# Kernel tuning notes

Hardware: AMD Instinct MI355X
Metric: run time of the kernel (lower is better)

Reference implementation:

```python
import jax, jax.numpy as jnp
import numpy as np

D_MODEL = 1024
N_HEAD = 16
D_K = D_MODEL // N_HEAD


def setup_inputs() -> dict:
    key = jax.random.key(0)
    k1, k2, k3 = jax.random.split(key, 3)
    B, S = 2, 2048
    x = jax.random.normal(k1, (B, S, D_MODEL), dtype=jnp.float32)
    attention_mask = jnp.ones((B, 1, 1, S), dtype=jnp.float32)
    # Conv1D params: weight [nx, nf], bias [nf]; init std=0.02 per source
    W_attn = 0.02 * jax.random.normal(k2, (D_MODEL, 3 * D_MODEL), dtype=jnp.float32)
    b_attn = jnp.zeros((3 * D_MODEL,), dtype=jnp.float32)
    W_proj = 0.02 * jax.random.normal(k3, (D_MODEL, D_MODEL), dtype=jnp.float32)
    b_proj = jnp.zeros((D_MODEL,), dtype=jnp.float32)
    return {"x": x, "attention_mask": attention_mask,
            "W_attn": W_attn, "b_attn": b_attn,
            "W_proj": W_proj, "b_proj": b_proj}


def reference(x, attention_mask, W_attn, b_attn, W_proj, b_proj):
    B, S, _ = x.shape
    # c_attn: fused QKV projection (Conv1D == addmm)
    qkv = x @ W_attn + b_attn                       # [B, S, 3*D]
    q, k, v = jnp.split(qkv, 3, axis=-1)            # each [B, S, D]

    def split_heads(t):                             # [B, S, D] -> [B, H, S, d_k]
        return t.reshape(B, S, N_HEAD, D_K).transpose(0, 2, 1, 3)

    q, k, v = split_heads(q), split_heads(k), split_heads(v)
    scale = 1.0 / jnp.sqrt(jnp.float32(D_K))
    scores = jnp.einsum("bhqd,bhkd->bhqk", q, k) * scale   # [B, H, S, S]
    scores = scores + (1.0 - attention_mask) * -10000.0
    scores = jax.nn.softmax(scores, axis=-1)
    # dropout omitted (eval / deterministic)
    out = jnp.einsum("bhqk,bhkd->bhqd", scores, v)          # [B, H, S, d_k]
    out = out.transpose(0, 2, 1, 3).reshape(B, S, D_MODEL)  # merge heads
    out = out @ W_proj + b_proj                             # c_proj
    return out, scores
```

## Files before the change

### kernel.cpp

```cpp
#include <hip/hip_runtime.h>

typedef unsigned short u16;
typedef __bf16 bf16x8 __attribute__((ext_vector_type(8)));
typedef float f32x4 __attribute__((ext_vector_type(4)));

#define D_MODEL 1024
#define S_LEN 2048
#define NH 16
#define DK 64
#define BATCH 2
#define M_ROWS (BATCH * S_LEN)
#define NQKV (3 * D_MODEL)

__device__ __forceinline__ u16 f2bf(float x) {
  union { __bf16 h; u16 u; } v; v.h = (__bf16)x;
  return v.u;
}
__device__ __forceinline__ float bf2f(u16 b) {
  union { unsigned u; float f; } v; v.u = ((unsigned)b) << 16; return v.f;
}
__device__ __forceinline__ void gload16(const void* g, void* l) {
  __builtin_amdgcn_global_load_lds((const __attribute__((address_space(1))) unsigned int*)g,
                                   (__attribute__((address_space(3))) unsigned int*)l, 16, 0, 0);
}

__global__ __launch_bounds__(256) void pack_bf16(const float* __restrict__ in, u16* __restrict__ out) {
  const int idx = (blockIdx.x * 256 + threadIdx.x) * 8;
  float4 a = *(const float4*)&in[idx];
  float4 b = *(const float4*)&in[idx + 4];
  unsigned p0 = (unsigned)f2bf(a.x) | ((unsigned)f2bf(a.y) << 16);
  unsigned p1 = (unsigned)f2bf(a.z) | ((unsigned)f2bf(a.w) << 16);
  unsigned p2 = (unsigned)f2bf(b.x) | ((unsigned)f2bf(b.y) << 16);
  unsigned p3 = (unsigned)f2bf(b.z) | ((unsigned)f2bf(b.w) << 16);
  int4 o; o.x = (int)p0; o.y = (int)p1; o.z = (int)p2; o.w = (int)p3;
  *(int4*)&out[idx] = o;
}

__global__ __launch_bounds__(256) void transpose_pack(const float* __restrict__ in, u16* __restrict__ out,
                                                      int R, int C) {
  __shared__ u16 T[64][68];
  const int r0 = blockIdx.x * 64, c0 = blockIdx.y * 64;
  const int t = threadIdx.x;
  const int col = t & 63, rq = t >> 6;
#pragma unroll
  for (int s = 0; s < 16; ++s) {
    int row = s * 4 + rq;
    T[col][row] = f2bf(in[(size_t)(r0 + row) * C + c0 + col]);
  }
  __syncthreads();
#pragma unroll
  for (int s = 0; s < 16; ++s) {
    int crow = s * 4 + rq;
    out[(size_t)(c0 + crow) * R + r0 + col] = T[crow][col];
  }
}

template <int OUTF32>
__global__ __launch_bounds__(256) void gemm_bt(const u16* __restrict__ A, const u16* __restrict__ BT,
                                               const float* __restrict__ bias, void* __restrict__ outp,
                                               int K, int N) {
  __shared__ u16 As[2][128 * 64];
  __shared__ u16 Bs[2][128 * 64];
  const int m0 = blockIdx.x * 128, n0 = blockIdx.y * 128;
  const int t = threadIdx.x, lane = t & 63, w = t >> 6;
  const int wr = w >> 1, wc = w & 1;
  const int l15 = lane & 15, l4 = lane >> 4;
  const int srow = lane >> 3, schunk = lane & 7;

  f32x4 acc[4][4] = {};

#define STAGE_G(buf, k0)                                                        \
  do {                                                                          \
    _Pragma("unroll") for (int i = 0; i < 4; ++i) {                             \
      int r0 = (i * 4 + w) * 8;                                                 \
      int r = r0 + srow;                                                        \
      int sc = (schunk ^ (r & 7)) * 8;                                          \
      gload16(&A[(size_t)(m0 + r) * K + (k0) + sc], &As[buf][r0 * 64]);         \
      gload16(&BT[(size_t)(n0 + r) * K + (k0) + sc], &Bs[buf][r0 * 64]);        \
    }                                                                           \
  } while (0)

  STAGE_G(0, 0);
  __syncthreads();
  const int nk = K / 64;
  int cur = 0;
  for (int t0 = 0; t0 < nk; ++t0) {
    if (t0 + 1 < nk) STAGE_G(cur ^ 1, (t0 + 1) * 64);
#pragma unroll
    for (int ks = 0; ks < 2; ++ks) {
      bf16x8 af[4], bfr[4];
#pragma unroll
      for (int g = 0; g < 4; ++g) {
        int ra = wr * 64 + g * 16 + l15;
        int rb = wc * 64 + g * 16 + l15;
        af[g]  = *(const bf16x8*)&As[cur][ra * 64 + ((ks * 4 + l4) ^ (ra & 7)) * 8];
        bfr[g] = *(const bf16x8*)&Bs[cur][rb * 64 + ((ks * 4 + l4) ^ (rb & 7)) * 8];
      }
#pragma unroll
      for (int mg = 0; mg < 4; ++mg)
#pragma unroll
        for (int ng = 0; ng < 4; ++ng)
          acc[mg][ng] = __builtin_amdgcn_mfma_f32_16x16x32_bf16(af[mg], bfr[ng], acc[mg][ng], 0, 0, 0);
    }
    __syncthreads();
    cur ^= 1;
  }
#undef STAGE_G
  const int rowb = m0 + wr * 64, colb = n0 + wc * 64;
#pragma unroll
  for (int mg = 0; mg < 4; ++mg)
#pragma unroll
    for (int ng = 0; ng < 4; ++ng) {
      int col = colb + ng * 16 + l15;
      float bv = bias[col];
#pragma unroll
      for (int j = 0; j < 4; ++j) {
        int row = rowb + mg * 16 + l4 * 4 + j;
        float val = acc[mg][ng][j] + bv;
        if (OUTF32) ((float*)outp)[(size_t)row * N + col] = val;
        else        ((u16*)outp)[(size_t)row * N + col] = f2bf(val);
      }
    }
}

__global__ __launch_bounds__(512, 6) void attn_fused(const u16* __restrict__ qkv, const float* __restrict__ mask,
                                                     float* __restrict__ scores, u16* __restrict__ attnout) {
  __shared__ u16 Ks[2][64 * 64];
  __shared__ u16 Vt[2][64 * 68];
  __shared__ u16 Ps[8][16][40];
  __shared__ float RS[4][16][2];
  const int bid = blockIdx.x;
  const int qt = bid & 31, h = (bid >> 5) & 15, b = bid >> 9;
  const int t = threadIdx.x, lane = t & 63, w = t >> 6;
  const int qg = w >> 1, kg = w & 1;
  const int l15 = lane & 15, l4 = lane >> 4;
  const u16* kbase = qkv + (size_t)b * S_LEN * NQKV + D_MODEL + h * DK;
  const u16* vbase = kbase + D_MODEL;
  const float* mrow = mask + b * S_LEN;

  bf16x8 qf[2];
  {
    const int qrow = qt * 64 + qg * 16 + l15;
    const u16* qp = qkv + (size_t)(b * S_LEN + qrow) * NQKV + h * DK;
#pragma unroll
    for (int ks = 0; ks < 2; ++ks) {
      union { bf16x8 v; u16 s[8]; } qa;
      qa.v = *(const bf16x8*)&qp[ks * 32 + l4 * 8];
#pragma unroll
      for (int e = 0; e < 8; ++e) qa.s[e] = f2bf(bf2f(qa.s[e]) * 0.125f);
      qf[ks] = qa.v;
    }
  }

  const int krow = t >> 3;
  const int kchunk = ((t & 7) ^ (krow & 7)) * 8;
#define STAGE_K(buf, kt) \
  gload16(&kbase[(size_t)((kt) * 64 + krow) * NQKV + kchunk], &Ks[buf][w * 512])

  float ps4[4] = {0.f, 0.f, 0.f, 0.f};
  int cur = 0;
  STAGE_K(0, 0);
  __syncthreads();
  for (int kt = 0; kt < 32; ++kt) {
    if (kt + 1 < 32) STAGE_K(cur ^ 1, kt + 1);
    f32x4 sacc[2] = {};
#pragma unroll
    for (int ks = 0; ks < 2; ++ks) {
      bf16x8 kf[2];
#pragma unroll
      for (int n = 0; n < 2; ++n) {
        int kr = kg * 32 + n * 16 + l15;
        kf[n] = *(const bf16x8*)&Ks[cur][kr * 64 + ((ks * 4 + l4) ^ (kr & 7)) * 8];
      }
#pragma unroll
      for (int n = 0; n < 2; ++n)
        sacc[n] = __builtin_amdgcn_mfma_f32_16x16x32_bf16(qf[ks], kf[n], sacc[n], 0, 0, 0);
    }
#pragma unroll
    for (int n = 0; n < 2; ++n) {
      float m = mrow[kt * 64 + kg * 32 + n * 16 + l15];
      float mb = -10000.0f * (1.0f - m);
#pragma unroll
      for (int j = 0; j < 4; ++j) ps4[j] += __expf(sacc[n][j] + mb);
    }
    __syncthreads();
    cur ^= 1;
  }
#pragma unroll
  for (int off = 1; off < 16; off <<= 1)
#pragma unroll
    for (int j = 0; j < 4; ++j) ps4[j] += __shfl_xor(ps4[j], off, 64);
  if (l15 == 0)
#pragma unroll
    for (int j = 0; j < 4; ++j) RS[qg][l4 * 4 + j][kg] = ps4[j];
  __syncthreads();
  float inv4[4];
#pragma unroll
  for (int j = 0; j < 4; ++j) inv4[j] = 1.0f / (RS[qg][l4 * 4 + j][0] + RS[qg][l4 * 4 + j][1]);

  f32x4 oacc[4] = {};
  const int vr = t >> 3, vc = (t & 7) * 8;
  const size_t sbase = ((size_t)((b * NH + h) * S_LEN + qt * 64 + qg * 16 + l4 * 4)) * S_LEN + l15;

  STAGE_K(0, 0);
  {
    const u16* vp = &vbase[(size_t)vr * NQKV + vc];
    int4 va0 = *(const int4*)vp;
    const u16* s0 = (const u16*)&va0;
#pragma unroll
    for (int i = 0; i < 8; ++i) Vt[0][(vc + i) * 68 + vr] = s0[i];
  }
  __syncthreads();
  cur = 0;
  for (int kt = 0; kt < 32; ++kt) {
    const bool hn = (kt + 1 < 32);
    int4 va;
    if (hn) {
      STAGE_K(cur ^ 1, kt + 1);
      va = *(const int4*)&vbase[(size_t)((kt + 1) * 64 + vr) * NQKV + vc];
    }
    f32x4 sacc[2] = {};
#pragma unroll
    for (int ks = 0; ks < 2; ++ks) {
      bf16x8 kf[2];
#pragma unroll
      for (int n = 0; n < 2; ++n) {
        int kr = kg * 32 + n * 16 + l15;
        kf[n] = *(const bf16x8*)&Ks[cur][kr * 64 + ((ks * 4 + l4) ^ (kr & 7)) * 8];
      }
#pragma unroll
      for (int n = 0; n < 2; ++n)
        sacc[n] = __builtin_amdgcn_mfma_f32_16x16x32_bf16(qf[ks], kf[n], sacc[n], 0, 0, 0);
    }
#pragma unroll
    for (int n = 0; n < 2; ++n) {
      float m = mrow[kt * 64 + kg * 32 + n * 16 + l15];
      float mb = -10000.0f * (1.0f - m);
#pragma unroll
      for (int j = 0; j < 4; ++j) {
        float p = __expf(sacc[n][j] + mb) * inv4[j];
        scores[sbase + (size_t)j * S_LEN + kt * 64 + kg * 32 + n * 16] = p;
        Ps[w][l4 * 4 + j][n * 16 + l15] = f2bf(p);
      }
    }
    {
      bf16x8 pa = *(const bf16x8*)&Ps[w][l15][l4 * 8];
      bf16x8 vf[4];
#pragma unroll
      for (int dn = 0; dn < 4; ++dn)
        vf[dn] = *(const bf16x8*)&Vt[cur][(dn * 16 + l15) * 68 + kg * 32 + l4 * 8];
#pragma unroll
      for (int dn = 0; dn < 4; ++dn)
        oacc[dn] = __builtin_amdgcn_mfma_f32_16x16x32_bf16(pa, vf[dn], oacc[dn], 0, 0, 0);
    }
    if (hn) {
      const u16* s0 = (const u16*)&va;
#pragma unroll
      for (int i = 0; i < 8; ++i) Vt[cur ^ 1][(vc + i) * 68 + vr] = s0[i];
    }
    __syncthreads();
    cur ^= 1;
  }
#undef STAGE_K
  float* OX = (float*)&Ks[0][0];
  if (kg == 1) {
#pragma unroll
    for (int dn = 0; dn < 4; ++dn)
#pragma unroll
      for (int j = 0; j < 4; ++j)
        OX[(qg * 16 + l4 * 4 + j) * 64 + dn * 16 + l15] = oacc[dn][j];
  }
  __syncthreads();
  if (kg == 0) {
#pragma unroll
    for (int dn = 0; dn < 4; ++dn) {
      int col = h * DK + dn * 16 + l15;
#pragma unroll
      for (int j = 0; j < 4; ++j) {
        int row = b * S_LEN + qt * 64 + qg * 16 + l4 * 4 + j;
        float o = oacc[dn][j] + OX[(qg * 16 + l4 * 4 + j) * 64 + dn * 16 + l15];
        attnout[(size_t)row * D_MODEL + col] = f2bf(o);
      }
    }
  }
}

extern "C" void kernel_launch(void* const* d_in, const int* in_sizes, int n_in,
                              void* d_out, int out_size, void* d_ws, size_t ws_size,
                              hipStream_t stream) {
  const float* x      = (const float*)d_in[0];
  const float* mask   = (const float*)d_in[1];
  const float* W_attn = (const float*)d_in[2];
  const float* b_attn = (const float*)d_in[3];
  const float* W_proj = (const float*)d_in[4];
  const float* b_proj = (const float*)d_in[5];
  float* out    = (float*)d_out;
  float* scores = out + (size_t)M_ROWS * D_MODEL;

  char* ws = (char*)d_ws;
  u16* xb     = (u16*)ws;
  u16* wqkvT  = (u16*)(ws + (size_t)(8  << 20));
  u16* wprojT = (u16*)(ws + (size_t)(14 << 20));
  u16* qkv    = (u16*)(ws + (size_t)(16 << 20));
  u16* attnb  = (u16*)(ws + (size_t)(40 << 20));

  pack_bf16<<<(M_ROWS * D_MODEL) / (256 * 8), 256, 0, stream>>>(x, xb);
  transpose_pack<<<dim3(D_MODEL / 64, NQKV / 64), 256, 0, stream>>>(W_attn, wqkvT, D_MODEL, NQKV);
  transpose_pack<<<dim3(D_MODEL / 64, D_MODEL / 64), 256, 0, stream>>>(W_proj, wprojT, D_MODEL, D_MODEL);
  gemm_bt<0><<<dim3(M_ROWS / 128, NQKV / 128), 256, 0, stream>>>(xb, wqkvT, b_attn, (void*)qkv, D_MODEL, NQKV);
  attn_fused<<<BATCH * NH * (S_LEN / 64), 512, 0, stream>>>(qkv, mask, scores, attnb);
  gemm_bt<1><<<dim3(M_ROWS / 128, D_MODEL / 128), 256, 0, stream>>>(attnb, wprojT, b_proj, (void*)out, D_MODEL, D_MODEL);
}
```

Before: 287.4 us.

## Double attention query tile per block, precompute mask bias in LDS

Each attention block now handles 128 query rows instead of 64, with each wave computing two 16-row MFMA groups. This halves the number of K/V tile loads and V transposes per query row. The mask bias is precomputed once into shared memory instead of being read from global memory every iteration. The end-of-loop __syncthreads is replaced with an explicit lgkmcnt wait plus a raw barrier. In exchange it uses more registers and LDS, lowers the occupancy target to 4, and halves the grid to 512 blocks.

```diff
diff --git a/kernel.cpp b/kernel.cpp
--- a/kernel.cpp
+++ b/kernel.cpp
@@ -123,24 +123,33 @@
     }
 }
 
-__global__ __launch_bounds__(512, 6) void attn_fused(const u16* __restrict__ qkv, const float* __restrict__ mask,
+__global__ __launch_bounds__(512, 4) void attn_fused(const u16* __restrict__ qkv, const float* __restrict__ mask,
                                                      float* __restrict__ scores, u16* __restrict__ attnout) {
   __shared__ u16 Ks[2][64 * 64];
   __shared__ u16 Vt[2][64 * 68];
-  __shared__ u16 Ps[8][16][40];
-  __shared__ float RS[4][16][2];
+  __shared__ u16 Ps[8][32][40];
+  __shared__ float MB[S_LEN];
+  __shared__ float RS[4][32][2];
   const int bid = blockIdx.x;
-  const int qt = bid & 31, h = (bid >> 5) & 15, b = bid >> 9;
+  const int qt = bid & 15, h = (bid >> 4) & 15, b = bid >> 8;
   const int t = threadIdx.x, lane = t & 63, w = t >> 6;
   const int qg = w >> 1, kg = w & 1;
   const int l15 = lane & 15, l4 = lane >> 4;
   const u16* kbase = qkv + (size_t)b * S_LEN * NQKV + D_MODEL + h * DK;
   const u16* vbase = kbase + D_MODEL;
-  const float* mrow = mask + b * S_LEN;
-
-  bf16x8 qf[2];
+
   {
-    const int qrow = qt * 64 + qg * 16 + l15;
+    float4 m4 = *(const float4*)&mask[b * S_LEN + t * 4];
+    MB[t * 4 + 0] = -10000.0f * (1.0f - m4.x);
+    MB[t * 4 + 1] = -10000.0f * (1.0f - m4.y);
+    MB[t * 4 + 2] = -10000.0f * (1.0f - m4.z);
+    MB[t * 4 + 3] = -10000.0f * (1.0f - m4.w);
+  }
+
+  bf16x8 qf[2][2];
+#pragma unroll
+  for (int mg = 0; mg < 2; ++mg) {
+    const int qrow = qt * 128 + qg * 32 + mg * 16 + l15;
     const u16* qp = qkv + (size_t)(b * S_LEN + qrow) * NQKV + h * DK;
 #pragma unroll
     for (int ks = 0; ks < 2; ++ks) {
@@ -148,22 +157,22 @@
       qa.v = *(const bf16x8*)&qp[ks * 32 + l4 * 8];
 #pragma unroll
       for (int e = 0; e < 8; ++e) qa.s[e] = f2bf(bf2f(qa.s[e]) * 0.125f);
-      qf[ks] = qa.v;
-    }
-  }
-
-  const int krow = t >> 3;
-  const int kchunk = ((t & 7) ^ (krow & 7)) * 8;
+      qf[mg][ks] = qa.v;
+    }
+  }
+
+  const int krow = w * 8 + (lane >> 3);
+  const int kchunk = ((lane & 7) ^ (krow & 7)) * 8;
 #define STAGE_K(buf, kt) \
   gload16(&kbase[(size_t)((kt) * 64 + krow) * NQKV + kchunk], &Ks[buf][w * 512])
 
-  float ps4[4] = {0.f, 0.f, 0.f, 0.f};
+  float ps4[2][4] = {};
   int cur = 0;
   STAGE_K(0, 0);
   __syncthreads();
   for (int kt = 0; kt < 32; ++kt) {
     if (kt + 1 < 32) STAGE_K(cur ^ 1, kt + 1);
-    f32x4 sacc[2] = {};
+    f32x4 sacc[2][2] = {};
 #pragma unroll
     for (int ks = 0; ks < 2; ++ks) {
       bf16x8 kf[2];
@@ -173,15 +182,18 @@
         kf[n] = *(const bf16x8*)&Ks[cur][kr * 64 + ((ks * 4 + l4) ^ (kr & 7)) * 8];
       }
 #pragma unroll
-      for (int n = 0; n < 2; ++n)
-        sacc[n] = __builtin_amdgcn_mfma_f32_16x16x32_bf16(qf[ks], kf[n], sacc[n], 0, 0, 0);
+      for (int mg = 0; mg < 2; ++mg)
+#pragma unroll
+        for (int n = 0; n < 2; ++n)
+          sacc[mg][n] = __builtin_amdgcn_mfma_f32_16x16x32_bf16(qf[mg][ks], kf[n], sacc[mg][n], 0, 0, 0);
     }
 #pragma unroll
     for (int n = 0; n < 2; ++n) {
-      float m = mrow[kt * 64 + kg * 32 + n * 16 + l15];
-      float mb = -10000.0f * (1.0f - m);
-#pragma unroll
-      for (int j = 0; j < 4; ++j) ps4[j] += __expf(sacc[n][j] + mb);
+      float mb = MB[kt * 64 + kg * 32 + n * 16 + l15];
+#pragma unroll
+      for (int mg = 0; mg < 2; ++mg)
+#pragma unroll
+        for (int j = 0; j < 4; ++j) ps4[mg][j] += __expf(sacc[mg][n][j] + mb);
     }
     __syncthreads();
     cur ^= 1;
@@ -189,18 +201,31 @@
 #pragma unroll
   for (int off = 1; off < 16; off <<= 1)
 #pragma unroll
-    for (int j = 0; j < 4; ++j) ps4[j] += __shfl_xor(ps4[j], off, 64);
+    for (int mg = 0; mg < 2; ++mg)
+#pragma unroll
+      for (int j = 0; j < 4; ++j) ps4[mg][j] += __shfl_xor(ps4[mg][j], off, 64);
   if (l15 == 0)
 #pragma unroll
-    for (int j = 0; j < 4; ++j) RS[qg][l4 * 4 + j][kg] = ps4[j];
-  __syncthreads();
-  float inv4[4];
-#pragma unroll
-  for (int j = 0; j < 4; ++j) inv4[j] = 1.0f / (RS[qg][l4 * 4 + j][0] + RS[qg][l4 * 4 + j][1]);
-
-  f32x4 oacc[4] = {};
+    for (int mg = 0; mg < 2; ++mg)
+#pragma unroll
+      for (int j = 0; j < 4; ++j) RS[qg][mg * 16 + l4 * 4 + j][kg] = ps4[mg][j];
+  __syncthreads();
+  float inv4[2][4];
+#pragma unroll
+  for (int mg = 0; mg < 2; ++mg)
+#pragma unroll
+    for (int j = 0; j < 4; ++j) {
+      int r = mg * 16 + l4 * 4 + j;
+      inv4[mg][j] = 1.0f / (RS[qg][r][0] + RS[qg][r][1]);
+    }
+
+  f32x4 oacc[2][4] = {};
   const int vr = t >> 3, vc = (t & 7) * 8;
-  const size_t sbase = ((size_t)((b * NH + h) * S_LEN + qt * 64 + qg * 16 + l4 * 4)) * S_LEN + l15;
+  size_t sb[2];
+#pragma unroll
+  for (int mg = 0; mg < 2; ++mg)
+    sb[mg] = ((size_t)((b * NH + h) * S_LEN + qt * 128 + qg * 32 + mg * 16 + l4 * 4)) * S_LEN
+             + kg * 32 + l15;
 
   STAGE_K(0, 0);
   {
@@ -219,7 +244,7 @@
       STAGE_K(cur ^ 1, kt + 1);
       va = *(const int4*)&vbase[(size_t)((kt + 1) * 64 + vr) * NQKV + vc];
     }
-    f32x4 sacc[2] = {};
+    f32x4 sacc[2][2] = {};
 #pragma unroll
     for (int ks = 0; ks < 2; ++ks) {
       bf16x8 kf[2];
@@ -229,59 +254,75 @@
         kf[n] = *(const bf16x8*)&Ks[cur][kr * 64 + ((ks * 4 + l4) ^ (kr & 7)) * 8];
       }
 #pragma unroll
-      for (int n = 0; n < 2; ++n)
-        sacc[n] = __builtin_amdgcn_mfma_f32_16x16x32_bf16(qf[ks], kf[n], sacc[n], 0, 0, 0);
+      for (int mg = 0; mg < 2; ++mg)
+#pragma unroll
+        for (int n = 0; n < 2; ++n)
+          sacc[mg][n] = __builtin_amdgcn_mfma_f32_16x16x32_bf16(qf[mg][ks], kf[n], sacc[mg][n], 0, 0, 0);
     }
 #pragma unroll
     for (int n = 0; n < 2; ++n) {
-      float m = mrow[kt * 64 + kg * 32 + n * 16 + l15];
-      float mb = -10000.0f * (1.0f - m);
-#pragma unroll
-      for (int j = 0; j < 4; ++j) {
-        float p = __expf(sacc[n][j] + mb) * inv4[j];
-        scores[sbase + (size_t)j * S_LEN + kt * 64 + kg * 32 + n * 16] = p;
-        Ps[w][l4 * 4 + j][n * 16 + l15] = f2bf(p);
-      }
+      float mb = MB[kt * 64 + kg * 32 + n * 16 + l15];
+#pragma unroll
+      for (int mg = 0; mg < 2; ++mg)
+#pragma unroll
+        for (int j = 0; j < 4; ++j) {
+          float p = __expf(sacc[mg][n][j] + mb) * inv4[mg][j];
+          scores[sb[mg] + (size_t)j * S_LEN + kt * 64 + n * 16] = p;
+          Ps[w][mg * 16 + l4 * 4 + j][n * 16 + l15] = f2bf(p);
+        }
     }
     {
-      bf16x8 pa = *(const bf16x8*)&Ps[w][l15][l4 * 8];
-      bf16x8 vf[4];
+      bf16x8 pa[2], vf[4];
+#pragma unroll
+      for (int mg = 0; mg < 2; ++mg)
+        pa[mg] = *(const bf16x8*)&Ps[w][mg * 16 + l15][l4 * 8];
 #pragma unroll
       for (int dn = 0; dn < 4; ++dn)
         vf[dn] = *(const bf16x8*)&Vt[cur][(dn * 16 + l15) * 68 + kg * 32 + l4 * 8];
 #pragma unroll
-      for (int dn = 0; dn < 4; ++dn)
-        oacc[dn] = __builtin_amdgcn_mfma_f32_16x16x32_bf16(pa, vf[dn], oacc[dn], 0, 0, 0);
+      for (int mg = 0; mg < 2; ++mg)
+#pragma unroll
+        for (int dn = 0; dn < 4; ++dn)
+          oacc[mg][dn] = __builtin_amdgcn_mfma_f32_16x16x32_bf16(pa[mg], vf[dn], oacc[mg][dn], 0, 0, 0);
     }
     if (hn) {
       const u16* s0 = (const u16*)&va;
 #pragma unroll
       for (int i = 0; i < 8; ++i) Vt[cur ^ 1][(vc + i) * 68 + vr] = s0[i];
     }
-    __syncthreads();
+    asm volatile("s_waitcnt lgkmcnt(0)" ::: "memory");
+    __builtin_amdgcn_s_barrier();
     cur ^= 1;
   }
 #undef STAGE_K
-  float* OX = (float*)&Ks[0][0];
+  __syncthreads();
   if (kg == 1) {
 #pragma unroll
-    for (int dn = 0; dn < 4; ++dn)
-#pragma unroll
-      for (int j = 0; j < 4; ++j)
-        OX[(qg * 16 + l4 * 4 + j) * 64 + dn * 16 + l15] = oacc[dn][j];
+    for (int mg = 0; mg < 2; ++mg)
+#pragma unroll
+      for (int dn = 0; dn < 4; ++dn)
+#pragma unroll
+        for (int j = 0; j < 4; ++j) {
+          int r = qg * 32 + mg * 16 + l4 * 4 + j;
+          float* base = (r < 64) ? (float*)&Ks[0][0] : (float*)&Vt[0][0];
+          base[(r & 63) * 64 + dn * 16 + l15] = oacc[mg][dn][j];
+        }
   }
   __syncthreads();
   if (kg == 0) {
 #pragma unroll
-    for (int dn = 0; dn < 4; ++dn) {
-      int col = h * DK + dn * 16 + l15;
-#pragma unroll
-      for (int j = 0; j < 4; ++j) {
-        int row = b * S_LEN + qt * 64 + qg * 16 + l4 * 4 + j;
-        float o = oacc[dn][j] + OX[(qg * 16 + l4 * 4 + j) * 64 + dn * 16 + l15];
-        attnout[(size_t)row * D_MODEL + col] = f2bf(o);
-      }
-    }
+    for (int mg = 0; mg < 2; ++mg)
+#pragma unroll
+      for (int dn = 0; dn < 4; ++dn) {
+        int col = h * DK + dn * 16 + l15;
+#pragma unroll
+        for (int j = 0; j < 4; ++j) {
+          int r = qg * 32 + mg * 16 + l4 * 4 + j;
+          const float* base = (r < 64) ? (const float*)&Ks[0][0] : (const float*)&Vt[0][0];
+          float o = oacc[mg][dn][j] + base[(r & 63) * 64 + dn * 16 + l15];
+          attnout[(size_t)(b * S_LEN + qt * 128 + r) * D_MODEL + col] = f2bf(o);
+        }
+      }
   }
 }
 
@@ -308,6 +349,6 @@
   transpose_pack<<<dim3(D_MODEL / 64, NQKV / 64), 256, 0, stream>>>(W_attn, wqkvT, D_MODEL, NQKV);
   transpose_pack<<<dim3(D_MODEL / 64, D_MODEL / 64), 256, 0, stream>>>(W_proj, wprojT, D_MODEL, D_MODEL);
   gemm_bt<0><<<dim3(M_ROWS / 128, NQKV / 128), 256, 0, stream>>>(xb, wqkvT, b_attn, (void*)qkv, D_MODEL, NQKV);
-  attn_fused<<<BATCH * NH * (S_LEN / 64), 512, 0, stream>>>(qkv, mask, scores, attnb);
+  attn_fused<<<BATCH * NH * (S_LEN / 128), 512, 0, stream>>>(qkv, mask, scores, attnb);
   gemm_bt<1><<<dim3(M_ROWS / 128, D_MODEL / 128), 256, 0, stream>>>(attnb, wprojT, b_proj, (void*)out, D_MODEL, D_MODEL);
 }
```

Result: faster. 268.3 us (-6.6%).
